# Optimization experiments

Hardware: AMD Instinct MI355X
Metric: run time of the kernel (lower is better)

The kernel has to match this reference:

```python
import jax, jax.numpy as jnp
import numpy as np

OUTERCUTOFF = 5.0  # seqm_parameters['pair_outer_cutoff']
LENGTH_CONV = 1.8897261258369282  # Angstrom -> Bohr (constants.length_conversion_factor)
NMOL, MOLSIZE = 1024, 128


def setup_inputs() -> dict:
    key = jax.random.key(0)
    k1, k2 = jax.random.split(key)
    species = jax.random.randint(k1, (NMOL, MOLSIZE), 0, 9).astype(jnp.int32)
    coordinates = jax.random.uniform(k2, (NMOL, MOLSIZE, 3), dtype=jnp.float32) * 20.0
    # core charges indexed by atomic number (0=blank, H=1, ..., F=9)
    tore = jnp.array([0.0, 1.0, 0.0, 1.0, 2.0, 3.0, 4.0, 5.0, 6.0, 7.0], dtype=jnp.float32)
    return {"species": species, "coordinates": coordinates, "tore": tore}


def reference(species, coordinates, tore):
    nmol, molsize = species.shape
    nonblank = species > 0                               # (nmol, molsize)
    flat_nb = nonblank.reshape(-1)
    atom_index = jnp.arange(nmol * molsize, dtype=jnp.int32)
    real_atoms = atom_index[flat_nb]                     # compaction (eager, data-dependent)
    n_real = real_atoms.shape[0]
    inv_real_atoms = jnp.zeros((nmol * molsize,), jnp.int32).at[real_atoms].set(
        jnp.arange(n_real, dtype=jnp.int32))
    Z = species.reshape(-1)[real_atoms]
    nHeavy = jnp.sum(species > 1, axis=1)
    nHydro = jnp.sum(species == 1, axis=1)
    nocc = (jnp.sum(tore[species], axis=1) / 2.0).reshape(-1).astype(jnp.int32)
    t1 = (jnp.arange(molsize, dtype=jnp.int32) * (molsize + 1))[None, :]
    t2 = (jnp.arange(nmol, dtype=jnp.int32) * molsize ** 2)[:, None]
    maskd = (t1 + t2).reshape(-1)[real_atoms]
    atom_molid = jnp.repeat(jnp.arange(nmol, dtype=jnp.int32), molsize)[flat_nb]
    # pair bookkeeping: [i, a, b] with first=atom a, second=atom b
    nonblank_pairs = (nonblank[:, None, :] & nonblank[:, :, None]).reshape(-1)
    ai = atom_index.reshape(nmol, molsize)
    pair_first = jnp.broadcast_to(ai[:, :, None], (nmol, molsize, molsize)).reshape(-1)
    pair_second = jnp.broadcast_to(ai[:, None, :], (nmol, molsize, molsize)).reshape(-1)
    # paircoord_raw[i, a, b] = coord[i, b] - coord[i, a]
    paircoord_raw = (coordinates[:, None, :, :] - coordinates[:, :, None, :]).reshape(-1, 3)
    pairdist_raw = jnp.linalg.norm(paircoord_raw, axis=1)
    close_pairs = pairdist_raw < OUTERCUTOFF
    pairs = (pair_first < pair_second) & nonblank_pairs & close_pairs
    pidx = jnp.where(pairs)[0]
    paircoord = paircoord_raw[pidx]
    pairdist = pairdist_raw[pidx]
    rij = pairdist * LENGTH_CONV
    idxi = inv_real_atoms[pair_first[pidx]]
    idxj = inv_real_atoms[pair_second[pidx]]
    ni = Z[idxi]
    nj = Z[idxj]
    xij = paircoord / pairdist[:, None]
    mask = real_atoms[idxi] * molsize + real_atoms[idxj] % molsize
    pair_molid = atom_molid[idxi]
    return (nmol, molsize, nHeavy, nHydro, nocc, Z, maskd, atom_molid,
            mask, pair_molid, ni, nj, idxi, idxj, xij, rij)
```

## Files before the change

kernel.cpp:

```cpp
#include <hip/hip_runtime.h>
#include <hip/hip_bf16.h>

#define NMOL 1024
#define MOLSIZE 128


__device__ __forceinline__ float pair_dist(float ax, float ay, float az,
                                           float bx, float by, float bz,
                                           float& dx, float& dy, float& dz) {
    dx = __fsub_rn(bx, ax);
    dy = __fsub_rn(by, ay);
    dz = __fsub_rn(bz, az);
    float d2 = __fadd_rn(__fadd_rn(__fmul_rn(dx, dx), __fmul_rn(dy, dy)), __fmul_rn(dz, dz));
    return __fsqrt_rn(d2);
}

__global__ __launch_bounds__(256) void k_count(const int* __restrict__ species,
                                               const float* __restrict__ coord,
                                               const float* __restrict__ tore,
                                               float* __restrict__ out,
                                               int* __restrict__ cnt_real,
                                               int* __restrict__ pair_tot,
                                               unsigned long long* __restrict__ bal_g) {
    __shared__ float cx[MOLSIZE], cy[MOLSIZE], cz[MOLSIZE];
    __shared__ unsigned long long bal_s[256];
    __shared__ int sH[2], sY[2], sN[2];
    __shared__ float sT[2];
    __shared__ int wpair[4];
    int m = blockIdx.x, t = threadIdx.x;
    int lane = t & 63, w = t >> 6;
    if (t < MOLSIZE) {
        int f = m * MOLSIZE + t;
        int s = species[f];
        bool nb = (s > 0);
        float x = coord[f * 3 + 0], y = coord[f * 3 + 1], z = coord[f * 3 + 2];
        float sent = 1.0e30f * (float)(t + 1);
        cx[t] = nb ? x : sent;
        cy[t] = nb ? y : sent;
        cz[t] = nb ? z : sent;
        int h = (s > 1) ? 1 : 0, yy = (s == 1) ? 1 : 0, nn = nb ? 1 : 0;
        float tv = tore[s];
        for (int d = 32; d > 0; d >>= 1) {
            h += __shfl_down(h, d);
            yy += __shfl_down(yy, d);
            nn += __shfl_down(nn, d);
            tv += __shfl_down(tv, d);
        }
        if (lane == 0) { sH[w] = h; sY[w] = yy; sN[w] = nn; sT[w] = tv; }
    }
    __syncthreads();
    if (t == 0) {
        out[2 + m] = (float)(sH[0] + sH[1]);
        out[2 + NMOL + m] = (float)(sY[0] + sY[1]);
        out[2 + 2 * NMOL + m] = (float)((int)((sT[0] + sT[1]) * 0.5f));
        cnt_real[m] = sN[0] + sN[1];
        if (m == 0) { out[0] = (float)NMOL; out[1] = (float)MOLSIZE; }
    }
    float bxl = cx[lane], byl = cy[lane], bzl = cz[lane];
    float bxh = cx[64 + lane], byh = cy[64 + lane], bzh = cz[64 + lane];
    int wcount = 0;
    for (int j = 0; j < 32; ++j) {
        int a = w + 4 * j;
        float ax = cx[a], ay = cy[a], az = cz[a];
        unsigned long long mb0 = 0ull, mb1 = 0ull;
        if (a < 63) {
            float dx, dy, dz;
            float dist = pair_dist(ax, ay, az, bxl, byl, bzl, dx, dy, dz);
            mb0 = __ballot((lane > a) && (dist < 5.0f));
        }
        if (a < 127) {
            float dx, dy, dz;
            float dist = pair_dist(ax, ay, az, bxh, byh, bzh, dx, dy, dz);
            mb1 = __ballot(((64 + lane) > a) && (dist < 5.0f));
        }
        if (lane == 0) { bal_s[2 * a] = mb0; bal_s[2 * a + 1] = mb1; }
        wcount += __popcll(mb0) + __popcll(mb1);
    }
    if (lane == 0) wpair[w] = wcount;
    __syncthreads();
    if (t == 0) pair_tot[m] = wpair[0] + wpair[1] + wpair[2] + wpair[3];
    bal_g[m * 256 + t] = bal_s[t];
}

__global__ void k_scan2(const int* __restrict__ cnt_real, const int* __restrict__ pair_tot,
                        int* __restrict__ mol_base, int* __restrict__ pair_mol_base) {
    const int* cnt = blockIdx.x ? pair_tot : cnt_real;
    int* base = blockIdx.x ? pair_mol_base : mol_base;
    __shared__ int wt[4];
    int t = threadIdx.x, lane = t & 63, w = t >> 6;
    int v0 = cnt[t * 4 + 0], v1 = cnt[t * 4 + 1], v2 = cnt[t * 4 + 2], v3 = cnt[t * 4 + 3];
    int s = v0 + v1 + v2 + v3;
    int v = s;
    for (int d = 1; d < 64; d <<= 1) {
        int u = __shfl_up(v, d);
        if (lane >= d) v += u;
    }
    if (lane == 63) wt[w] = v;
    __syncthreads();
    int add = 0;
    for (int ww = 0; ww < w; ++ww) add += wt[ww];
    int incl = v + add;
    int excl = incl - s;
    base[t * 4 + 0] = excl;
    base[t * 4 + 1] = excl + v0;
    base[t * 4 + 2] = excl + v0 + v1;
    base[t * 4 + 3] = excl + v0 + v1 + v2;
    if (t == 255) base[1024] = incl;
}

__global__ __launch_bounds__(256) void k_scatter(const int* __restrict__ species,
                                                 const float* __restrict__ coord,
                                                 const int* __restrict__ mol_base,
                                                 const int* __restrict__ pair_mol_base,
                                                 const unsigned long long* __restrict__ bal_g,
                                                 float* __restrict__ out) {
    __shared__ float cx[MOLSIZE], cy[MOLSIZE], cz[MOLSIZE], spf[MOLSIZE];
    __shared__ int iv[MOLSIZE];
    __shared__ unsigned long long bal_s[256];
    __shared__ int sIncl[256];
    __shared__ int wtot[4];
    __shared__ int wc0s;
    int m = blockIdx.x, t = threadIdx.x;
    int lane = t & 63, w = t >> 6;
    int n_real = mol_base[NMOL];
    int npairs = pair_mol_base[NMOL];

    unsigned long long bal = bal_g[m * 256 + t];
    bal_s[t] = bal;
    int cval = __popcll(bal);

    int s_at = 0;
    unsigned long long amb = 0ull;
    if (t < MOLSIZE) {
        int f = m * MOLSIZE + t;
        s_at = species[f];
        cx[t] = coord[f * 3 + 0];
        cy[t] = coord[f * 3 + 1];
        cz[t] = coord[f * 3 + 2];
        spf[t] = (float)s_at;
        amb = __ballot(s_at > 0);
        if (t == 0) wc0s = __popcll(amb);
    }
    int v = cval;
    for (int d = 1; d < 64; d <<= 1) {
        int u = __shfl_up(v, d);
        if (lane >= d) v += u;
    }
    if (lane == 63) wtot[w] = v;
    __syncthreads();
    if (t < MOLSIZE && s_at > 0) {
        int rank = __popcll(amb & ((1ull << lane) - 1ull)) + ((w == 1) ? wc0s : 0);
        int g = mol_base[m] + rank;
        iv[t] = g;
        out[3074 + g] = (float)s_at;
        out[3074 + n_real + g] = (float)(t * (MOLSIZE + 1) + m * (MOLSIZE * MOLSIZE));
        out[3074 + 2 * n_real + g] = (float)m;
    }
    int add = 0;
    for (int ww = 0; ww < w; ++ww) add += wtot[ww];
    int np_mol = wtot[0] + wtot[1] + wtot[2] + wtot[3];
    sIncl[t] = v + add;
    __syncthreads();

    int offP = 3074 + 3 * n_real;
    float* pm0 = out + offP;
    float* pm1 = pm0 + npairs;
    float* pm2 = pm1 + npairs;
    float* pm3 = pm2 + npairs;
    float* pm4 = pm3 + npairs;
    float* pm5 = pm4 + npairs;
    float* px  = pm5 + npairs;
    float* pr  = px + 3 * npairs;
    int qbase = pair_mol_base[m];
    float fm = (float)m;

    for (int q = t; q < np_mol; q += 256) {
        int c = 0;
        if (sIncl[c + 127] <= q) c += 128;
        if (sIncl[c + 63] <= q) c += 64;
        if (sIncl[c + 31] <= q) c += 32;
        if (sIncl[c + 15] <= q) c += 16;
        if (sIncl[c + 7] <= q) c += 8;
        if (sIncl[c + 3] <= q) c += 4;
        if (sIncl[c + 1] <= q) c += 2;
        if (sIncl[c] <= q) c += 1;
        int r = q - (c ? sIncl[c - 1] : 0);
        unsigned long long mb = bal_s[c];
        unsigned int cur = (unsigned int)mb;
        int idx = 0;
        int cc = __popc(cur);
        if (r >= cc) { r -= cc; idx = 32; cur = (unsigned int)(mb >> 32); }
        cc = __popc(cur & 0xFFFFu); if (r >= cc) { r -= cc; idx += 16; cur >>= 16; }
        cc = __popc(cur & 0xFFu);   if (r >= cc) { r -= cc; idx += 8;  cur >>= 8; }
        cc = __popc(cur & 0xFu);    if (r >= cc) { r -= cc; idx += 4;  cur >>= 4; }
        cc = __popc(cur & 0x3u);    if (r >= cc) { r -= cc; idx += 2;  cur >>= 2; }
        cc = cur & 1u;              if (r >= cc) { idx += 1; }
        int a = c >> 1;
        int b = ((c & 1) << 6) | idx;
        float dx, dy, dz;
        float dist = pair_dist(cx[a], cy[a], cz[a], cx[b], cy[b], cz[b], dx, dy, dz);
        int Q = qbase + q;
        pm0[Q] = (float)(m * (MOLSIZE * MOLSIZE) + a * MOLSIZE + b);
        pm1[Q] = fm;
        pm2[Q] = spf[a];
        pm3[Q] = spf[b];
        pm4[Q] = (float)iv[a];
        pm5[Q] = (float)iv[b];
        px[3 * Q + 0] = __fdiv_rn(dx, dist);
        px[3 * Q + 1] = __fdiv_rn(dy, dist);
        px[3 * Q + 2] = __fdiv_rn(dz, dist);
        pr[Q] = __fmul_rn(dist, 1.8897261258369282f);
    }
}

extern "C" void kernel_launch(void* const* d_in, const int* in_sizes, int n_in,
                              void* d_out, int out_size, void* d_ws, size_t ws_size,
                              hipStream_t stream) {
    const int* species = (const int*)d_in[0];
    const float* coords = (const float*)d_in[1];
    const float* tore = (const float*)d_in[2];
    float* out = (float*)d_out;
    int* ws = (int*)d_ws;

    int* cnt_real      = ws;
    int* pair_tot      = ws + 1024;
    int* mol_base      = ws + 2048;
    int* pair_mol_base = ws + 3073;
    unsigned long long* bal_g = (unsigned long long*)(ws + 4100);

    k_count<<<NMOL, 256, 0, stream>>>(species, coords, tore, out, cnt_real, pair_tot, bal_g);
    k_scan2<<<2, 256, 0, stream>>>(cnt_real, pair_tot, mol_base, pair_mol_base);
    k_scatter<<<NMOL, 256, 0, stream>>>(species, coords, mol_base, pair_mol_base, bal_g, out);
}
```

Measured before the change: 81.30 us.

## Fuse count, scan and scatter kernels into one cooperative kernel with grid syncs

The three separate kernels (per-molecule count, two-block prefix scan, scatter) become a single cooperative kernel separated by two grid-wide syncs. Shared-memory state from the count phase (coordinates, pair ballots, species) is kept for the scatter phase, so the ballot masks no longer take a round trip through global memory and nothing is reloaded. This removes two kernel-launch boundaries. In exchange it needs all 1024 blocks resident at once, adds grid-barrier cost, and the scan runs on only two blocks while the rest of the grid waits.

```diff
diff --git a/kernel.cpp b/kernel.cpp
--- a/kernel.cpp
+++ b/kernel.cpp
@@ -1,5 +1,8 @@
 #include <hip/hip_runtime.h>
 #include <hip/hip_bf16.h>
+#include <hip/hip_cooperative_groups.h>
+
+namespace cg = cooperative_groups;
 
 #define NMOL 1024
 #define MOLSIZE 128
@@ -15,31 +18,43 @@
     return __fsqrt_rn(d2);
 }
 
-__global__ __launch_bounds__(256) void k_count(const int* __restrict__ species,
+__global__ __launch_bounds__(256) void k_fused(const int* __restrict__ species,
                                                const float* __restrict__ coord,
                                                const float* __restrict__ tore,
                                                float* __restrict__ out,
                                                int* __restrict__ cnt_real,
                                                int* __restrict__ pair_tot,
-                                               unsigned long long* __restrict__ bal_g) {
-    __shared__ float cx[MOLSIZE], cy[MOLSIZE], cz[MOLSIZE];
+                                               int* __restrict__ mol_base,
+                                               int* __restrict__ pair_mol_base) {
+    cg::grid_group grid = cg::this_grid();
+    __shared__ float cx[MOLSIZE], cy[MOLSIZE], cz[MOLSIZE], spf[MOLSIZE];
+    __shared__ int iv[MOLSIZE];
     __shared__ unsigned long long bal_s[256];
+    __shared__ int sIncl[256];
     __shared__ int sH[2], sY[2], sN[2];
     __shared__ float sT[2];
-    __shared__ int wpair[4];
+    __shared__ int wpair[4], wt[4], wtot[4];
+    __shared__ int wc0s;
+
     int m = blockIdx.x, t = threadIdx.x;
     int lane = t & 63, w = t >> 6;
+
+    int s_at = 0;
+    unsigned long long amb = 0ull;
     if (t < MOLSIZE) {
         int f = m * MOLSIZE + t;
-        int s = species[f];
-        bool nb = (s > 0);
-        float x = coord[f * 3 + 0], y = coord[f * 3 + 1], z = coord[f * 3 + 2];
+        s_at = species[f];
+        bool nb = (s_at > 0);
+        float x = coord[3 * f + 0], y = coord[3 * f + 1], z = coord[3 * f + 2];
         float sent = 1.0e30f * (float)(t + 1);
         cx[t] = nb ? x : sent;
         cy[t] = nb ? y : sent;
         cz[t] = nb ? z : sent;
-        int h = (s > 1) ? 1 : 0, yy = (s == 1) ? 1 : 0, nn = nb ? 1 : 0;
-        float tv = tore[s];
+        spf[t] = (float)s_at;
+        amb = __ballot(nb);
+        if (t == 0) wc0s = __popcll(amb);
+        int h = (s_at > 1) ? 1 : 0, yy = (s_at == 1) ? 1 : 0, nn = nb ? 1 : 0;
+        float tv = tore[s_at];
         for (int d = 32; d > 0; d >>= 1) {
             h += __shfl_down(h, d);
             yy += __shfl_down(yy, d);
@@ -79,68 +94,36 @@
     if (lane == 0) wpair[w] = wcount;
     __syncthreads();
     if (t == 0) pair_tot[m] = wpair[0] + wpair[1] + wpair[2] + wpair[3];
-    bal_g[m * 256 + t] = bal_s[t];
-}
-
-__global__ void k_scan2(const int* __restrict__ cnt_real, const int* __restrict__ pair_tot,
-                        int* __restrict__ mol_base, int* __restrict__ pair_mol_base) {
-    const int* cnt = blockIdx.x ? pair_tot : cnt_real;
-    int* base = blockIdx.x ? pair_mol_base : mol_base;
-    __shared__ int wt[4];
-    int t = threadIdx.x, lane = t & 63, w = t >> 6;
-    int v0 = cnt[t * 4 + 0], v1 = cnt[t * 4 + 1], v2 = cnt[t * 4 + 2], v3 = cnt[t * 4 + 3];
-    int s = v0 + v1 + v2 + v3;
-    int v = s;
-    for (int d = 1; d < 64; d <<= 1) {
-        int u = __shfl_up(v, d);
-        if (lane >= d) v += u;
-    }
-    if (lane == 63) wt[w] = v;
-    __syncthreads();
-    int add = 0;
-    for (int ww = 0; ww < w; ++ww) add += wt[ww];
-    int incl = v + add;
-    int excl = incl - s;
-    base[t * 4 + 0] = excl;
-    base[t * 4 + 1] = excl + v0;
-    base[t * 4 + 2] = excl + v0 + v1;
-    base[t * 4 + 3] = excl + v0 + v1 + v2;
-    if (t == 255) base[1024] = incl;
-}
-
-__global__ __launch_bounds__(256) void k_scatter(const int* __restrict__ species,
-                                                 const float* __restrict__ coord,
-                                                 const int* __restrict__ mol_base,
-                                                 const int* __restrict__ pair_mol_base,
-                                                 const unsigned long long* __restrict__ bal_g,
-                                                 float* __restrict__ out) {
-    __shared__ float cx[MOLSIZE], cy[MOLSIZE], cz[MOLSIZE], spf[MOLSIZE];
-    __shared__ int iv[MOLSIZE];
-    __shared__ unsigned long long bal_s[256];
-    __shared__ int sIncl[256];
-    __shared__ int wtot[4];
-    __shared__ int wc0s;
-    int m = blockIdx.x, t = threadIdx.x;
-    int lane = t & 63, w = t >> 6;
+    __threadfence();
+    grid.sync();
+
+    if (m < 2) {
+        const int* cnt = m ? pair_tot : cnt_real;
+        int* base = m ? pair_mol_base : mol_base;
+        int v0 = cnt[4 * t + 0], v1 = cnt[4 * t + 1], v2 = cnt[4 * t + 2], v3 = cnt[4 * t + 3];
+        int s = v0 + v1 + v2 + v3;
+        int v = s;
+        for (int d = 1; d < 64; d <<= 1) {
+            int u = __shfl_up(v, d);
+            if (lane >= d) v += u;
+        }
+        if (lane == 63) wt[w] = v;
+        __syncthreads();
+        int add = 0;
+        for (int ww = 0; ww < w; ++ww) add += wt[ww];
+        int incl = v + add, excl = incl - s;
+        base[4 * t + 0] = excl;
+        base[4 * t + 1] = excl + v0;
+        base[4 * t + 2] = excl + v0 + v1;
+        base[4 * t + 3] = excl + v0 + v1 + v2;
+        if (t == 255) base[1024] = incl;
+        __threadfence();
+    }
+    grid.sync();
+
     int n_real = mol_base[NMOL];
     int npairs = pair_mol_base[NMOL];
-
-    unsigned long long bal = bal_g[m * 256 + t];
-    bal_s[t] = bal;
-    int cval = __popcll(bal);
-
-    int s_at = 0;
-    unsigned long long amb = 0ull;
-    if (t < MOLSIZE) {
-        int f = m * MOLSIZE + t;
-        s_at = species[f];
-        cx[t] = coord[f * 3 + 0];
-        cy[t] = coord[f * 3 + 1];
-        cz[t] = coord[f * 3 + 2];
-        spf[t] = (float)s_at;
-        amb = __ballot(s_at > 0);
-        if (t == 0) wc0s = __popcll(amb);
-    }
+    int cval = __popcll(bal_s[t]);
     int v = cval;
     for (int d = 1; d < 64; d <<= 1) {
         int u = __shfl_up(v, d);
@@ -158,9 +141,9 @@
     }
     int add = 0;
     for (int ww = 0; ww < w; ++ww) add += wtot[ww];
-    int np_mol = wtot[0] + wtot[1] + wtot[2] + wtot[3];
     sIncl[t] = v + add;
     __syncthreads();
+    int np_mol = sIncl[255];
 
     int offP = 3074 + 3 * n_real;
     float* pm0 = out + offP;
@@ -226,9 +209,8 @@
     int* pair_tot      = ws + 1024;
     int* mol_base      = ws + 2048;
     int* pair_mol_base = ws + 3073;
-    unsigned long long* bal_g = (unsigned long long*)(ws + 4100);
-
-    k_count<<<NMOL, 256, 0, stream>>>(species, coords, tore, out, cnt_real, pair_tot, bal_g);
-    k_scan2<<<2, 256, 0, stream>>>(cnt_real, pair_tot, mol_base, pair_mol_base);
-    k_scatter<<<NMOL, 256, 0, stream>>>(species, coords, mol_base, pair_mol_base, bal_g, out);
+
+    void* args[] = {(void*)&species, (void*)&coords, (void*)&tore, (void*)&out,
+                    (void*)&cnt_real, (void*)&pair_tot, (void*)&mol_base, (void*)&pair_mol_base};
+    hipLaunchCooperativeKernel((void*)k_fused, dim3(NMOL), dim3(256), args, 0, stream);
 }
```

Result: slower. 248.1 us (+205.1%).

## Fold prefix-scan kernel into scatter via per-block redundant reductions

Applied to the files above, without the earlier changes.

Removes the separate two-block scan kernel. Each scatter block now reads the full per-molecule atom and pair count arrays and reduces them itself to get its own base offset and the global totals. This saves one kernel launch and the serialized gap between launches. In exchange, every block does redundant reads and reductions over 1024 counts and adds a shared-memory reduction step before the scatter.

```diff
diff --git a/kernel.cpp b/kernel.cpp
--- a/kernel.cpp
+++ b/kernel.cpp
@@ -33,7 +33,7 @@
         int f = m * MOLSIZE + t;
         int s = species[f];
         bool nb = (s > 0);
-        float x = coord[f * 3 + 0], y = coord[f * 3 + 1], z = coord[f * 3 + 2];
+        float x = coord[3 * f + 0], y = coord[3 * f + 1], z = coord[3 * f + 2];
         float sent = 1.0e30f * (float)(t + 1);
         cx[t] = nb ? x : sent;
         cy[t] = nb ? y : sent;
@@ -82,36 +82,10 @@
     bal_g[m * 256 + t] = bal_s[t];
 }
 
-__global__ void k_scan2(const int* __restrict__ cnt_real, const int* __restrict__ pair_tot,
-                        int* __restrict__ mol_base, int* __restrict__ pair_mol_base) {
-    const int* cnt = blockIdx.x ? pair_tot : cnt_real;
-    int* base = blockIdx.x ? pair_mol_base : mol_base;
-    __shared__ int wt[4];
-    int t = threadIdx.x, lane = t & 63, w = t >> 6;
-    int v0 = cnt[t * 4 + 0], v1 = cnt[t * 4 + 1], v2 = cnt[t * 4 + 2], v3 = cnt[t * 4 + 3];
-    int s = v0 + v1 + v2 + v3;
-    int v = s;
-    for (int d = 1; d < 64; d <<= 1) {
-        int u = __shfl_up(v, d);
-        if (lane >= d) v += u;
-    }
-    if (lane == 63) wt[w] = v;
-    __syncthreads();
-    int add = 0;
-    for (int ww = 0; ww < w; ++ww) add += wt[ww];
-    int incl = v + add;
-    int excl = incl - s;
-    base[t * 4 + 0] = excl;
-    base[t * 4 + 1] = excl + v0;
-    base[t * 4 + 2] = excl + v0 + v1;
-    base[t * 4 + 3] = excl + v0 + v1 + v2;
-    if (t == 255) base[1024] = incl;
-}
-
 __global__ __launch_bounds__(256) void k_scatter(const int* __restrict__ species,
                                                  const float* __restrict__ coord,
-                                                 const int* __restrict__ mol_base,
-                                                 const int* __restrict__ pair_mol_base,
+                                                 const int* __restrict__ cnt_real,
+                                                 const int* __restrict__ pair_tot,
                                                  const unsigned long long* __restrict__ bal_g,
                                                  float* __restrict__ out) {
     __shared__ float cx[MOLSIZE], cy[MOLSIZE], cz[MOLSIZE], spf[MOLSIZE];
@@ -119,38 +93,61 @@
     __shared__ unsigned long long bal_s[256];
     __shared__ int sIncl[256];
     __shared__ int wtot[4];
+    __shared__ int redALT[4], redAALL[4], redPLT[4], redPALL[4];
     __shared__ int wc0s;
     int m = blockIdx.x, t = threadIdx.x;
     int lane = t & 63, w = t >> 6;
-    int n_real = mol_base[NMOL];
-    int npairs = pair_mol_base[NMOL];
 
     unsigned long long bal = bal_g[m * 256 + t];
     bal_s[t] = bal;
-    int cval = __popcll(bal);
+
+    int4 ca = ((const int4*)cnt_real)[t];
+    int4 cp = ((const int4*)pair_tot)[t];
+    int i0 = 4 * t;
+    int aLT = ((i0 + 0) < m ? ca.x : 0) + ((i0 + 1) < m ? ca.y : 0) +
+              ((i0 + 2) < m ? ca.z : 0) + ((i0 + 3) < m ? ca.w : 0);
+    int aALL = ca.x + ca.y + ca.z + ca.w;
+    int pLT = ((i0 + 0) < m ? cp.x : 0) + ((i0 + 1) < m ? cp.y : 0) +
+              ((i0 + 2) < m ? cp.z : 0) + ((i0 + 3) < m ? cp.w : 0);
+    int pALL = cp.x + cp.y + cp.z + cp.w;
+    for (int d = 32; d > 0; d >>= 1) {
+        aLT += __shfl_down(aLT, d);
+        aALL += __shfl_down(aALL, d);
+        pLT += __shfl_down(pLT, d);
+        pALL += __shfl_down(pALL, d);
+    }
+    if (lane == 0) { redALT[w] = aLT; redAALL[w] = aALL; redPLT[w] = pLT; redPALL[w] = pALL; }
 
     int s_at = 0;
     unsigned long long amb = 0ull;
     if (t < MOLSIZE) {
         int f = m * MOLSIZE + t;
         s_at = species[f];
-        cx[t] = coord[f * 3 + 0];
-        cy[t] = coord[f * 3 + 1];
-        cz[t] = coord[f * 3 + 2];
+        cx[t] = coord[3 * f + 0];
+        cy[t] = coord[3 * f + 1];
+        cz[t] = coord[3 * f + 2];
         spf[t] = (float)s_at;
         amb = __ballot(s_at > 0);
         if (t == 0) wc0s = __popcll(amb);
     }
-    int v = cval;
+    int v = __popcll(bal);
+    int cval = v;
     for (int d = 1; d < 64; d <<= 1) {
         int u = __shfl_up(v, d);
         if (lane >= d) v += u;
     }
+    (void)cval;
     if (lane == 63) wtot[w] = v;
     __syncthreads();
+
+    int mol_base_m = redALT[0] + redALT[1] + redALT[2] + redALT[3];
+    int n_real     = redAALL[0] + redAALL[1] + redAALL[2] + redAALL[3];
+    int qbase      = redPLT[0] + redPLT[1] + redPLT[2] + redPLT[3];
+    int npairs     = redPALL[0] + redPALL[1] + redPALL[2] + redPALL[3];
+
     if (t < MOLSIZE && s_at > 0) {
         int rank = __popcll(amb & ((1ull << lane) - 1ull)) + ((w == 1) ? wc0s : 0);
-        int g = mol_base[m] + rank;
+        int g = mol_base_m + rank;
         iv[t] = g;
         out[3074 + g] = (float)s_at;
         out[3074 + n_real + g] = (float)(t * (MOLSIZE + 1) + m * (MOLSIZE * MOLSIZE));
@@ -158,9 +155,9 @@
     }
     int add = 0;
     for (int ww = 0; ww < w; ++ww) add += wtot[ww];
-    int np_mol = wtot[0] + wtot[1] + wtot[2] + wtot[3];
     sIncl[t] = v + add;
     __syncthreads();
+    int np_mol = sIncl[255];
 
     int offP = 3074 + 3 * n_real;
     float* pm0 = out + offP;
@@ -171,7 +168,6 @@
     float* pm5 = pm4 + npairs;
     float* px  = pm5 + npairs;
     float* pr  = px + 3 * npairs;
-    int qbase = pair_mol_base[m];
     float fm = (float)m;
 
     for (int q = t; q < np_mol; q += 256) {
@@ -222,13 +218,10 @@
     float* out = (float*)d_out;
     int* ws = (int*)d_ws;
 
-    int* cnt_real      = ws;
-    int* pair_tot      = ws + 1024;
-    int* mol_base      = ws + 2048;
-    int* pair_mol_base = ws + 3073;
-    unsigned long long* bal_g = (unsigned long long*)(ws + 4100);
+    int* cnt_real = ws;
+    int* pair_tot = ws + 1024;
+    unsigned long long* bal_g = (unsigned long long*)(ws + 2048);
 
     k_count<<<NMOL, 256, 0, stream>>>(species, coords, tore, out, cnt_real, pair_tot, bal_g);
-    k_scan2<<<2, 256, 0, stream>>>(cnt_real, pair_tot, mol_base, pair_mol_base);
-    k_scatter<<<NMOL, 256, 0, stream>>>(species, coords, mol_base, pair_mol_base, bal_g, out);
-}
+    k_scatter<<<NMOL, 256, 0, stream>>>(species, coords, cnt_real, pair_tot, bal_g, out);
+}
```

Result: faster. 79.37 us (-2.4%).
